# Kernel optimization log

Hardware: AMD Instinct MI355X
Metric: run time of the kernel (lower is better)

The kernel has to match this reference:

```python
import jax, jax.numpy as jnp
import numpy as np

DIM = 256      # channel dim
NW = 7         # n_win per side
HEADS = 8
TOPK = 4
KVW = 4        # kv_per_win (ada_avgpool output side)
EPS = 1e-6


def _dwconv(x, w, b):
    # depthwise conv, NHWC, 'SAME' == padding k//2 for odd kernels
    y = jax.lax.conv_general_dilated(
        x, w, (1, 1), 'SAME',
        dimension_numbers=('NHWC', 'HWIO', 'NHWC'),
        feature_group_count=x.shape[-1])
    return y + b


def _ln(x, g, b):
    mu = x.mean(-1, keepdims=True)
    var = ((x - mu) ** 2).mean(-1, keepdims=True)
    return (x - mu) * jax.lax.rsqrt(var + EPS) * g + b


def _bra(x, qkv_w, qkv_b, wo_w, wo_b, lepe_w, lepe_b):
    # BiLevelRoutingAttention, x: (n, H, W, C)
    n, H, W, C = x.shape
    hw, ww = H // NW, W // NW          # window size (8, 8)
    scale = C ** -0.5                   # qk_dim ** -0.5 (BiFormer uses full qk_dim)
    qkv = x @ qkv_w.T + qkv_b           # (n, H, W, 3C)
    # window partition: n (j hw) (i ww) c -> n (j i) hw ww c
    qkv_win = qkv.reshape(n, NW, hw, NW, ww, 3 * C)
    qkv_win = qkv_win.transpose(0, 1, 3, 2, 4, 5).reshape(n, NW * NW, hw, ww, 3 * C)
    q = qkv_win[..., :C]                # (n, p2, hw, ww, C)
    kv = qkv_win[..., C:]               # (n, p2, hw, ww, 2C)
    # --- window-level routing (q/k detached in torch; no fwd effect) ---
    q_win = q.mean((2, 3))              # (n, p2, C)
    k_win = kv[..., :C].mean((2, 3))    # (n, p2, C)
    logits = jnp.einsum('npc,nqc->npq', q_win * scale, k_win)
    _, idx = jax.lax.top_k(logits, TOPK)            # (n, p2, k)
    # --- kv downsample: adaptive avg pool (hw,ww)->(KVW,KVW), exact 2x2 mean here ---
    fh, fw = hw // KVW, ww // KVW
    kv_pix = kv.reshape(n, NW * NW, KVW, fh, KVW, fw, 2 * C).mean((3, 5))
    kv_pix = kv_pix.reshape(n, NW * NW, KVW * KVW, 2 * C)   # (n, p2, w2, 2C)
    # --- gather top-k windows' kv ---
    kv_sel = jax.vmap(lambda t, ix: t[ix])(kv_pix, idx)     # (n, p2, k, w2, 2C)
    cph = C // HEADS
    k_sel = kv_sel[..., :C].reshape(n, NW * NW, TOPK * KVW * KVW, HEADS, cph)
    v_sel = kv_sel[..., C:].reshape(n, NW * NW, TOPK * KVW * KVW, HEADS, cph)
    q_pix = q.reshape(n, NW * NW, hw * ww, HEADS, cph)
    # --- windowed attention over gathered tokens ---
    att = jnp.einsum('npqmc,npsmc->npmqs', q_pix * scale, k_sel)
    att = jax.nn.softmax(att, axis=-1)
    out = jnp.einsum('npmqs,npsmc->npqmc', att, v_sel)
    out = out.reshape(n, NW, NW, hw, ww, C).transpose(0, 1, 3, 2, 4, 5).reshape(n, H, W, C)
    # --- lepe: depthwise 5x5 on v over the full image ---
    v_img = qkv[..., 2 * C:]
    out = out + _dwconv(v_img, lepe_w, lepe_b)
    return out @ wo_w.T + wo_b


def setup_inputs() -> dict:
    key = jax.random.key(0)
    ks = jax.random.split(key, 8)
    C, s = DIM, 0.02
    p = {}
    p['x'] = jax.random.normal(ks[0], (16, C, 56, 56), jnp.float32)
    p['pos_w'] = jax.random.normal(ks[1], (3, 3, 1, C), jnp.float32) * s
    p['pos_b'] = jnp.zeros((C,), jnp.float32)
    p['ln1_g'] = jnp.ones((C,), jnp.float32)
    p['ln1_b'] = jnp.zeros((C,), jnp.float32)
    p['ln2_g'] = jnp.ones((C,), jnp.float32)
    p['ln2_b'] = jnp.zeros((C,), jnp.float32)
    p['qkv_w'] = jax.random.normal(ks[2], (3 * C, C), jnp.float32) * s
    p['qkv_b'] = jnp.zeros((3 * C,), jnp.float32)
    p['wo_w'] = jax.random.normal(ks[3], (C, C), jnp.float32) * s
    p['wo_b'] = jnp.zeros((C,), jnp.float32)
    p['lepe_w'] = jax.random.normal(ks[4], (5, 5, 1, C), jnp.float32) * s
    p['lepe_b'] = jnp.zeros((C,), jnp.float32)
    p['fc1_w'] = jax.random.normal(ks[5], (4 * C, C), jnp.float32) * s
    p['fc1_b'] = jnp.zeros((4 * C,), jnp.float32)
    p['fc2_w'] = jax.random.normal(ks[6], (C, 4 * C), jnp.float32) * s
    p['fc2_b'] = jnp.zeros((C,), jnp.float32)
    return p


def reference(x, pos_w, pos_b, ln1_g, ln1_b, ln2_g, ln2_b, qkv_w, qkv_b,
              wo_w, wo_b, lepe_w, lepe_b, fc1_w, fc1_b, fc2_w, fc2_b):
    xh = x.transpose(0, 2, 3, 1)                       # NCHW -> NHWC
    xh = xh + _dwconv(xh, pos_w, pos_b)                # pos embed (dw 3x3)
    xh = xh + _bra(_ln(xh, ln1_g, ln1_b), qkv_w, qkv_b, wo_w, wo_b, lepe_w, lepe_b)
    h = _ln(xh, ln2_g, ln2_b)
    h = jax.nn.gelu(h @ fc1_w.T + fc1_b, approximate=False)
    xh = xh + (h @ fc2_w.T + fc2_b)
    return xh.transpose(0, 3, 1, 2)                    # NHWC -> NCHW
```

## Files before the change

### kernel.cpp

```cpp
#include <hip/hip_runtime.h>
#include <math.h>

static constexpr int NIMG = 16;
static constexpr int TOK  = NIMG * 56 * 56;
static constexpr size_t TC = (size_t)TOK * 256;
static constexpr int PTOK = 784 * 16;

typedef __bf16 bf16x8 __attribute__((ext_vector_type(8)));
typedef float  f32x4  __attribute__((ext_vector_type(4)));

__device__ inline float bf2f(unsigned short u) {
  unsigned int i = ((unsigned int)u) << 16; float f; __builtin_memcpy(&f, &i, 4); return f;
}
__device__ inline unsigned short f2bf(float f) {
  unsigned int i; __builtin_memcpy(&i, &f, 4);
  unsigned int r = i + 0x7fffu + ((i >> 16) & 1u);
  return (unsigned short)(r >> 16);
}

__global__ __launch_bounds__(256) void nchw2nhwc(const float* __restrict__ x,
                                                 float* __restrict__ y) {
  __shared__ float T[32][37];
  int nh = blockIdx.z;
  int n = nh / 56, h = nh % 56;
  int c0 = blockIdx.y * 32, w0 = blockIdx.x * 32;
  int tid = threadIdx.x;
  int wlim = 56 - w0; if (wlim > 32) wlim = 32;
  {
    int ci = tid >> 3, w = (tid & 7) * 4;
    if (w < wlim) {
      f32x4 v = *(const f32x4*)&x[(((size_t)n * 256 + c0 + ci) * 56 + h) * 56 + w0 + w];
#pragma unroll
      for (int j = 0; j < 4; j++) T[ci][w + j] = v[j];
    }
  }
  __syncthreads();
  {
    int wi = tid >> 3, cq = tid & 7;
    if (wi < wlim) {
      f32x4 o;
#pragma unroll
      for (int k = 0; k < 4; k++) o[k] = T[cq * 4 + k][wi];
      *(f32x4*)&y[(((size_t)n * 56 + h) * 56 + w0 + wi) * 256 + c0 + cq * 4] = o;
    }
  }
}

__global__ __launch_bounds__(256) void nhwc2nchw(const float* __restrict__ y,
                                                 float* __restrict__ o) {
  __shared__ float T[32][37];
  int nh = blockIdx.z;
  int n = nh / 56, h = nh % 56;
  int w0 = blockIdx.x * 32, c0 = blockIdx.y * 32;
  int tid = threadIdx.x;
  int wlim = 56 - w0; if (wlim > 32) wlim = 32;
  {
    int wi = tid >> 3, cq = tid & 7;
    if (wi < wlim) {
      f32x4 v = *(const f32x4*)&y[(((size_t)n * 56 + h) * 56 + w0 + wi) * 256 + c0 + cq * 4];
#pragma unroll
      for (int k = 0; k < 4; k++) T[wi][cq * 4 + k] = v[k];
    }
  }
  __syncthreads();
  {
    int ci = tid >> 3, w = (tid & 7) * 4;
    if (w < wlim) {
      f32x4 ov;
#pragma unroll
      for (int j = 0; j < 4; j++) ov[j] = T[w + j][ci];
      *(f32x4*)&o[(((size_t)n * 256 + c0 + ci) * 56 + h) * 56 + w0 + w] = ov;
    }
  }
}

__global__ __launch_bounds__(256) void posln_kernel(const float* __restrict__ xt,
                                                    const float* __restrict__ w,
                                                    const float* __restrict__ bb,
                                                    const float* __restrict__ g1,
                                                    const float* __restrict__ b1,
                                                    float* __restrict__ xh,
                                                    unsigned short* __restrict__ lnb,
                                                    float* __restrict__ murs) {
  int bid = blockIdx.x;
  int wgid = (bid & 7) * 1568 + (bid >> 3);
  int t = wgid * 4 + (threadIdx.x >> 6);
  int lane = threadIdx.x & 63;
  int c = lane * 4;
  int n = t / 3136, rem = t % 3136, h = rem / 56, ww = rem % 56;
  const float* base = xt + (size_t)n * 3136 * 256 + c;

  f32x4 xx[9]; float msk[9];
#pragma unroll
  for (int k = 0; k < 9; k++) {
    int dh = k / 3 - 1, dw = k % 3 - 1;
    int hh = h + dh, wc = ww + dw;
    msk[k] = ((unsigned)hh < 56u && (unsigned)wc < 56u) ? 1.f : 0.f;
    int hcl = hh < 0 ? 0 : (hh > 55 ? 55 : hh);
    int wcl = wc < 0 ? 0 : (wc > 55 ? 55 : wc);
    xx[k] = *(const f32x4*)&base[(size_t)(hcl * 56 + wcl) * 256];
  }
  f32x4 acc = *(const f32x4*)&bb[c];
#pragma unroll
  for (int k = 0; k < 9; k++) {
    f32x4 wv = *(const f32x4*)&w[k * 256 + c];
    acc += xx[k] * (wv * msk[k]);
  }
  f32x4 v = xx[4] + acc;
  *(f32x4*)&xh[(size_t)t * 256 + c] = v;

  float s = v[0] + v[1] + v[2] + v[3];
#pragma unroll
  for (int m = 1; m < 64; m <<= 1) s += __shfl_xor(s, m);
  float mu = s * (1.f / 256.f);
  f32x4 d = v - mu;
  float ss = d[0] * d[0] + d[1] * d[1] + d[2] * d[2] + d[3] * d[3];
#pragma unroll
  for (int m = 1; m < 64; m <<= 1) ss += __shfl_xor(ss, m);
  float rs = rsqrtf(ss * (1.f / 256.f) + 1e-6f);
  f32x4 gg = *(const f32x4*)&g1[c];
  f32x4 b4 = *(const f32x4*)&b1[c];
  f32x4 y = d * rs * gg + b4;
  unsigned short yb[4];
#pragma unroll
  for (int j = 0; j < 4; j++) yb[j] = f2bf(y[j]);
  __builtin_memcpy(lnb + (size_t)t * 256 + c, yb, 8);
  if (lane == 0) {
    murs[2 * (size_t)t] = mu;
    murs[2 * (size_t)t + 1] = rs;
  }
}

template <bool OUTBF, bool LN2F>
__global__ __launch_bounds__(512, 4) void mgemm2(const unsigned short* __restrict__ A, int lda,
                                                 const unsigned short* __restrict__ B, int ldb,
                                                 const float* __restrict__ bias,
                                                 const float* __restrict__ R,
                                                 void* __restrict__ C_,
                                                 int N, int K, int flags, int gx,
                                                 const float* __restrict__ g2,
                                                 const float* __restrict__ b2,
                                                 unsigned short* __restrict__ ob2) {
  __shared__ __attribute__((aligned(16))) char smraw[49152];
  unsigned short* As = (unsigned short*)smraw;
  unsigned short* Bs = (unsigned short*)(smraw + 16384);
  float* slab = (float*)smraw;
  constexpr int SSTR = 260;

  int tid = threadIdx.x;
  int nwg = gridDim.x, bid = blockIdx.x;
  int q8 = nwg >> 3, r8 = nwg & 7;
  int xcd = bid & 7, pos = bid >> 3;
  int wgid = (xcd < r8 ? xcd * (q8 + 1) : r8 * (q8 + 1) + (xcd - r8) * q8) + pos;
  int m0 = (wgid / gx) * 128;
  int n0 = (wgid % gx) * 256;

  int lane = tid & 63, wid = tid >> 6;
  int wr = (wid >> 2) * 64, wc = (wid & 3) * 64;
  int llo = lane & 15, lhi = lane >> 4;

  f32x4 acc[4][4];
#pragma unroll
  for (int i = 0; i < 4; i++)
#pragma unroll
    for (int j = 0; j < 4; j++) acc[i][j] = (f32x4){0.f, 0.f, 0.f, 0.f};

  for (int k0 = 0; k0 < K; k0 += 64) {
#pragma unroll
    for (int i = 0; i < 2; i++) {
      int qa = tid + 512 * i;
      int row = qa >> 3, col = (qa & 7) ^ (row & 7);
      __builtin_amdgcn_global_load_lds(
          (const __attribute__((address_space(1))) unsigned int*)
              (A + (size_t)(m0 + row) * lda + k0 + col * 8),
          (__attribute__((address_space(3))) unsigned int*)(As + qa * 8), 16, 0, 0);
    }
#pragma unroll
    for (int i = 0; i < 4; i++) {
      int qb = tid + 512 * i;
      int row = qb >> 3, col = (qb & 7) ^ (row & 7);
      __builtin_amdgcn_global_load_lds(
          (const __attribute__((address_space(1))) unsigned int*)
              (B + (size_t)(n0 + row) * ldb + k0 + col * 8),
          (__attribute__((address_space(3))) unsigned int*)(Bs + qb * 8), 16, 0, 0);
    }
    __syncthreads();
#pragma unroll
    for (int ks = 0; ks < 2; ks++) {
      int cchunk = ks * 4 + lhi;
      bf16x8 af[4], bfr[4];
#pragma unroll
      for (int mi = 0; mi < 4; mi++) {
        int r = wr + mi * 16 + llo;
        __builtin_memcpy(&af[mi], As + (size_t)r * 64 + (cchunk ^ (r & 7)) * 8, 16);
      }
#pragma unroll
      for (int nj = 0; nj < 4; nj++) {
        int r = wc + nj * 16 + llo;
        __builtin_memcpy(&bfr[nj], Bs + (size_t)r * 64 + (cchunk ^ (r & 7)) * 8, 16);
      }
#pragma unroll
      for (int mi = 0; mi < 4; mi++)
#pragma unroll
        for (int nj = 0; nj < 4; nj++)
          acc[mi][nj] = __builtin_amdgcn_mfma_f32_16x16x32_bf16(af[mi], bfr[nj],
                                                                acc[mi][nj], 0, 0, 0);
    }
    __syncthreads();
  }

#pragma unroll
  for (int s = 0; s < 4; s++) {
    if (wr == (s >> 1) * 64) {
#pragma unroll
      for (int mi2 = 0; mi2 < 2; mi2++) {
        int mi = (s & 1) * 2 + mi2;
#pragma unroll
        for (int nj = 0; nj < 4; nj++) {
          int col = wc + nj * 16 + llo;
#pragma unroll
          for (int j = 0; j < 4; j++)
            slab[(mi2 * 16 + lhi * 4 + j) * SSTR + col] = acc[mi][nj][j];
        }
      }
    }
    __syncthreads();
    int gmBase = m0 + s * 32;
    if (OUTBF) {
#pragma unroll
      for (int i2 = 0; i2 < 2; i2++) {
        int rr = wid * 4 + i2 * 2 + (lane >> 5);
        int col = (lane & 31) * 8;
        f32x4 v0 = *(f32x4*)&slab[rr * SSTR + col];
        f32x4 v1 = *(f32x4*)&slab[rr * SSTR + col + 4];
        if (!(flags & 8)) {
          v0 += *(const f32x4*)&bias[n0 + col];
          v1 += *(const f32x4*)&bias[n0 + col + 4];
        }
        if (flags & 1) {
#pragma unroll
          for (int j = 0; j < 4; j++) {
            v0[j] = 0.5f * v0[j] * (1.0f + erff(v0[j] * 0.70710678118654752f));
            v1[j] = 0.5f * v1[j] * (1.0f + erff(v1[j] * 0.70710678118654752f));
          }
        }
        unsigned short ob[8];
#pragma unroll
        for (int j = 0; j < 4; j++) { ob[j] = f2bf(v0[j]); ob[4 + j] = f2bf(v1[j]); }
        __builtin_memcpy((unsigned short*)C_ + (size_t)(gmBase + rr) * N + n0 + col, ob, 16);
      }
    } else {
#pragma unroll
      for (int i = 0; i < 4; i++) {
        int rr = wid * 4 + i;
        int gm = gmBase + rr;
        int col = lane * 4;
        f32x4 v = *(f32x4*)&slab[rr * SSTR + col];
        if (!(flags & 8)) v += *(const f32x4*)&bias[n0 + col];
        if (flags & 1) {
#pragma unroll
          for (int j = 0; j < 4; j++)
            v[j] = 0.5f * v[j] * (1.0f + erff(v[j] * 0.70710678118654752f));
        }
        if (flags & 2) v += *(const f32x4*)&R[(size_t)gm * N + n0 + col];
        if (LN2F) {
          float sv = v[0] + v[1] + v[2] + v[3];
          float qv = v[0] * v[0] + v[1] * v[1] + v[2] * v[2] + v[3] * v[3];
#pragma unroll
          for (int d = 1; d < 64; d <<= 1) {
            sv += __shfl_xor(sv, d);
            qv += __shfl_xor(qv, d);
          }
          float mu = sv * (1.f / 256.f);
          float var = qv * (1.f / 256.f) - mu * mu;
          float rs = rsqrtf(var + 1e-6f);
          f32x4 g4 = *(const f32x4*)&g2[col];
          f32x4 b4 = *(const f32x4*)&b2[col];
          f32x4 y = (v - mu) * rs * g4 + b4;
          unsigned short yb[4];
#pragma unroll
          for (int j = 0; j < 4; j++) yb[j] = f2bf(y[j]);
          __builtin_memcpy(ob2 + (size_t)gm * 256 + col, yb, 8);
        }
        *(f32x4*)&((float*)C_)[(size_t)gm * N + n0 + col] = v;
      }
    }
    __syncthreads();
  }
}

__global__ __launch_bounds__(256) void prep_kernel(const float* __restrict__ qkv_w,
                                                   const float* __restrict__ qkv_b,
                                                   const float* __restrict__ wo_w,
                                                   const float* __restrict__ fc1_w,
                                                   const float* __restrict__ fc2_w,
                                                   const float* __restrict__ lepe_w,
                                                   unsigned short* __restrict__ wqv,
                                                   unsigned short* __restrict__ wkv,
                                                   unsigned short* __restrict__ wwo,
                                                   unsigned short* __restrict__ wfc1,
                                                   unsigned short* __restrict__ wfc2,
                                                   float* __restrict__ bqv,
                                                   unsigned short* __restrict__ wlep) {
  int i = blockIdx.x * 256 + threadIdx.x;
  if (i < 65536) { wqv[i] = f2bf(qkv_w[i]); }
  else if (i < 131072) { int j = i - 65536; wqv[65536 + j] = f2bf(qkv_w[512 * 256 + j]); }
  else if (i < 262144) { int j = i - 131072; wkv[j] = f2bf(qkv_w[256 * 256 + j]); }
  else if (i < 327680) { int j = i - 262144; wwo[j] = f2bf(wo_w[j]); }
  else if (i < 589824) { int j = i - 327680; wfc1[j] = f2bf(fc1_w[j]); }
  else if (i < 851968) { int j = i - 589824; wfc2[j] = f2bf(fc2_w[j]); }
  else if (i < 852480) { int j = i - 851968; bqv[j] = qkv_b[j < 256 ? j : j + 256]; }
  else if (i < 858880) { int j = i - 852480; wlep[j] = f2bf(lepe_w[j]); }
}

__global__ __launch_bounds__(256) void pool_kernel(const float* __restrict__ xh,
                                                   const float* __restrict__ murs,
                                                   const float* __restrict__ g1,
                                                   const float* __restrict__ b1,
                                                   unsigned short* __restrict__ plx,
                                                   float* __restrict__ wmx) {
  int np = blockIdx.x * 4 + (threadIdx.x >> 6);
  int lane = threadIdx.x & 63;
  int c = lane * 4;
  int n = np / 49, p = np % 49, wr = p / 7, wcq = p % 7;
  f32x4 g4 = *(const f32x4*)&g1[c];
  f32x4 b4 = *(const f32x4*)&b1[c];
  f32x4 tot = (f32x4){0.f, 0.f, 0.f, 0.f};
  for (int s = 0; s < 16; s++) {
    int i = s >> 2, j = s & 3;
    f32x4 z = (f32x4){0.f, 0.f, 0.f, 0.f};
    for (int di = 0; di < 2; di++)
      for (int dj = 0; dj < 2; dj++) {
        size_t t = ((size_t)n * 56 + wr * 8 + i * 2 + di) * 56 + wcq * 8 + j * 2 + dj;
        float mu = murs[2 * t], rs = murs[2 * t + 1];
        f32x4 v = *(const f32x4*)&xh[t * 256 + c];
        z += (v - mu) * rs;
      }
    z *= 0.25f;
    f32x4 cell = z * g4 + b4;
    unsigned short ab[4];
#pragma unroll
    for (int k = 0; k < 4; k++) ab[k] = f2bf(cell[k]);
    __builtin_memcpy(plx + ((size_t)np * 16 + s) * 256 + c, ab, 8);
    tot += z;
  }
  f32x4 wm = tot * (1.f / 16.f) * g4 + b4;
  *(f32x4*)&wmx[(size_t)np * 256 + c] = wm;
}

__global__ __launch_bounds__(256) void winproj_kernel(const float* __restrict__ wmx,
                                                      const float* __restrict__ qkv_w,
                                                      const float* __restrict__ qkv_b,
                                                      float* __restrict__ qkwin) {
  int np = blockIdx.x, t = threadIdx.x;
  __shared__ float xs[256];
  xs[t] = wmx[(size_t)np * 256 + t];
  __syncthreads();
  for (int rep = 0; rep < 2; rep++) {
    int n = t + rep * 256;
    const float* wrow = qkv_w + (size_t)n * 256;
    float s = qkv_b[n];
    for (int c = 0; c < 256; c++) s += xs[c] * wrow[c];
    qkwin[(size_t)np * 512 + n] = s;
  }
}

__global__ __launch_bounds__(64) void topk_kernel(const float* __restrict__ qkwin,
                                                  int* __restrict__ idx) {
  int np = blockIdx.x;
  int n = np / 49;
  int j = threadIdx.x;
  __shared__ float lg[49];
  if (j < 49) {
    const float* qp = qkwin + (size_t)np * 512;
    const float* kp = qkwin + ((size_t)n * 49 + j) * 512 + 256;
    float s = 0.f;
    for (int c = 0; c < 256; c++) s += qp[c] * kp[c];
    lg[j] = s;
  }
  __syncthreads();
  if (j == 0) {
    unsigned long long used = 0ull;
    for (int t = 0; t < 4; t++) {
      float best = -INFINITY;
      int bi = 0;
      for (int q = 0; q < 49; q++)
        if (!((used >> q) & 1ull) && lg[q] > best) { best = lg[q]; bi = q; }
      idx[np * 4 + t] = bi;
      used |= (1ull << bi);
    }
  }
}

__global__ __launch_bounds__(64) void attn_mfma(const unsigned short* __restrict__ qvb,
                                                const unsigned short* __restrict__ kvp,
                                                const int* __restrict__ idx,
                                                unsigned short* __restrict__ out) {
  __shared__ unsigned short Vt[32 * 72];
  __shared__ unsigned short Pl[64 * 72];
  int bid = blockIdx.x;
  int head = bid & 7, np = bid >> 3;
  int n = np / 49, p = np % 49;
  int h0 = (p / 7) * 8, w0 = (p % 7) * 8;
  int lane = threadIdx.x;
  int lhi = lane >> 4, llo = lane & 15;

  int wi4[4];
#pragma unroll
  for (int t = 0; t < 4; t++) wi4[t] = idx[np * 4 + t];

#pragma unroll
  for (int it = 0; it < 4; it++) {
    int cell = lane >> 2;
    int chunk = lane & 3;
    int s = it * 16 + cell;
    const unsigned short* g = kvp + ((size_t)(n * 49 + wi4[it]) * 16 + cell) * 512
                              + 256 + head * 32 + chunk * 8;
    unsigned short vv[8];
    __builtin_memcpy(vv, g, 16);
#pragma unroll
    for (int j = 0; j < 8; j++) Vt[(chunk * 8 + j) * 72 + s] = vv[j];
  }

  bf16x8 qf[4], kf[4];
#pragma unroll
  for (int mi = 0; mi < 4; mi++) {
    int row = mi * 16 + llo;
    int h = h0 + (row >> 3), w = w0 + (row & 7);
    __builtin_memcpy(&qf[mi],
                     qvb + (((size_t)n * 56 + h) * 56 + w) * 512 + head * 32 + lhi * 8, 16);
  }
#pragma unroll
  for (int nj = 0; nj < 4; nj++) {
    __builtin_memcpy(&kf[nj],
                     kvp + ((size_t)(n * 49 + wi4[nj]) * 16 + llo) * 512 + head * 32 + lhi * 8,
                     16);
  }

  f32x4 acc[4][4];
#pragma unroll
  for (int mi = 0; mi < 4; mi++)
#pragma unroll
    for (int nj = 0; nj < 4; nj++) acc[mi][nj] = (f32x4){0.f, 0.f, 0.f, 0.f};
#pragma unroll
  for (int mi = 0; mi < 4; mi++)
#pragma unroll
    for (int nj = 0; nj < 4; nj++)
      acc[mi][nj] = __builtin_amdgcn_mfma_f32_16x16x32_bf16(qf[mi], kf[nj], acc[mi][nj], 0, 0, 0);

#pragma unroll
  for (int mi = 0; mi < 4; mi++)
#pragma unroll
    for (int nj = 0; nj < 4; nj++) acc[mi][nj] *= 0.0625f;
#pragma unroll
  for (int mi = 0; mi < 4; mi++) {
#pragma unroll
    for (int reg = 0; reg < 4; reg++) {
      float m = fmaxf(fmaxf(acc[mi][0][reg], acc[mi][1][reg]),
                      fmaxf(acc[mi][2][reg], acc[mi][3][reg]));
      m = fmaxf(m, __shfl_xor(m, 1));
      m = fmaxf(m, __shfl_xor(m, 2));
      m = fmaxf(m, __shfl_xor(m, 4));
      m = fmaxf(m, __shfl_xor(m, 8));
      float sum = 0.f;
#pragma unroll
      for (int nj = 0; nj < 4; nj++) {
        float e = __expf(acc[mi][nj][reg] - m);
        acc[mi][nj][reg] = e;
        sum += e;
      }
      sum += __shfl_xor(sum, 1);
      sum += __shfl_xor(sum, 2);
      sum += __shfl_xor(sum, 4);
      sum += __shfl_xor(sum, 8);
      float inv = 1.0f / sum;
#pragma unroll
      for (int nj = 0; nj < 4; nj++) acc[mi][nj][reg] *= inv;
    }
  }

#pragma unroll
  for (int mi = 0; mi < 4; mi++)
#pragma unroll
    for (int nj = 0; nj < 4; nj++)
#pragma unroll
      for (int reg = 0; reg < 4; reg++) {
        int row = mi * 16 + lhi * 4 + reg;
        Pl[row * 72 + nj * 16 + llo] = f2bf(acc[mi][nj][reg]);
      }

  f32x4 o[4][2];
#pragma unroll
  for (int mi = 0; mi < 4; mi++)
#pragma unroll
    for (int nc = 0; nc < 2; nc++) o[mi][nc] = (f32x4){0.f, 0.f, 0.f, 0.f};
#pragma unroll
  for (int ks = 0; ks < 2; ks++) {
    bf16x8 pa[4], vb[2];
#pragma unroll
    for (int mi = 0; mi < 4; mi++)
      __builtin_memcpy(&pa[mi], Pl + (mi * 16 + llo) * 72 + ks * 32 + lhi * 8, 16);
#pragma unroll
    for (int nc = 0; nc < 2; nc++)
      __builtin_memcpy(&vb[nc], Vt + (nc * 16 + llo) * 72 + ks * 32 + lhi * 8, 16);
#pragma unroll
    for (int mi = 0; mi < 4; mi++)
#pragma unroll
      for (int nc = 0; nc < 2; nc++)
        o[mi][nc] = __builtin_amdgcn_mfma_f32_16x16x32_bf16(pa[mi], vb[nc], o[mi][nc], 0, 0, 0);
  }

  __syncthreads();
#pragma unroll
  for (int mi = 0; mi < 4; mi++)
#pragma unroll
    for (int nc = 0; nc < 2; nc++)
#pragma unroll
      for (int reg = 0; reg < 4; reg++) {
        int row = mi * 16 + lhi * 4 + reg;
        Pl[row * 40 + nc * 16 + llo] = f2bf(o[mi][nc][reg]);
      }
  __syncthreads();
#pragma unroll
  for (int it = 0; it < 4; it++) {
    int slot = it * 64 + lane;
    int row = slot >> 2, cp = slot & 3;
    unsigned short ov[8];
    __builtin_memcpy(ov, Pl + row * 40 + cp * 8, 16);
    int h = h0 + (row >> 3), w = w0 + (row & 7);
    __builtin_memcpy(out + (((size_t)n * 56 + h) * 56 + w) * 256 + head * 32 + cp * 8, ov, 16);
  }
}

__global__ __launch_bounds__(256) void lepe_kernel(const unsigned short* __restrict__ qvb,
                                                   const unsigned short* __restrict__ wlep,
                                                   const float* __restrict__ b,
                                                   unsigned short* __restrict__ out) {
  __shared__ unsigned short Vs[60 * 272];
  int bid = blockIdx.x;
  int wgid = (bid & 7) * 784 + (bid >> 3);
  int tb = wgid * 8;
  int n = tb / 3136, rem = tb % 3136;
  int h0 = rem / 56, w0 = rem % 56;
  int tid = threadIdx.x;

  const unsigned short* vimg = qvb + (size_t)n * 3136 * 512 + 256;
  {
    int chunk = tid & 31;
    for (int s = tid >> 5; s < 60; s += 8) {
      int r = s / 12, cc = s % 12;
      int hh = h0 + r - 2; hh = hh < 0 ? 0 : (hh > 55 ? 55 : hh);
      int wcg = w0 + cc - 2; wcg = wcg < 0 ? 0 : (wcg > 55 ? 55 : wcg);
      unsigned short tmp[8];
      __builtin_memcpy(tmp, vimg + (size_t)(hh * 56 + wcg) * 512 + chunk * 8, 16);
      __builtin_memcpy(&Vs[s * 272 + chunk * 8], tmp, 16);
    }
  }
  __syncthreads();

  int px = tid >> 5;
  int cg = tid & 31;
  int c = cg * 8;
  int wq = w0 + px;

  float acc[8];
#pragma unroll
  for (int j = 0; j < 8; j++) acc[j] = b[c + j];

#pragma unroll
  for (int r = 0; r < 5; r++) {
    float hok = ((unsigned)(h0 + r - 2) < 56u) ? 1.f : 0.f;
#pragma unroll
    for (int dc = 0; dc < 5; dc++) {
      float m = hok * (((unsigned)(wq + dc - 2) < 56u) ? 1.f : 0.f);
      int slot = r * 12 + px + dc;
      unsigned short vv[8], wv[8];
      __builtin_memcpy(vv, &Vs[slot * 272 + cg * 8], 16);
      __builtin_memcpy(wv, wlep + (r * 5 + dc) * 256 + c, 16);
#pragma unroll
      for (int j = 0; j < 8; j++) acc[j] += bf2f(vv[j]) * (bf2f(wv[j]) * m);
    }
  }

  size_t o = (size_t)(tb + px) * 256 + c;
  unsigned short ov[8];
  __builtin_memcpy(ov, out + o, 16);
  unsigned short nv[8];
#pragma unroll
  for (int j = 0; j < 8; j++) nv[j] = f2bf(bf2f(ov[j]) + acc[j]);
  __builtin_memcpy(out + o, nv, 16);
}

extern "C" void kernel_launch(void* const* d_in, const int* in_sizes, int n_in,
                              void* d_out, int out_size, void* d_ws, size_t ws_size,
                              hipStream_t stream) {
  const float* x      = (const float*)d_in[0];
  const float* pos_w  = (const float*)d_in[1];
  const float* pos_b  = (const float*)d_in[2];
  const float* ln1_g  = (const float*)d_in[3];
  const float* ln1_b  = (const float*)d_in[4];
  const float* ln2_g  = (const float*)d_in[5];
  const float* ln2_b  = (const float*)d_in[6];
  const float* qkv_w  = (const float*)d_in[7];
  const float* qkv_b  = (const float*)d_in[8];
  const float* wo_w   = (const float*)d_in[9];
  const float* wo_b   = (const float*)d_in[10];
  const float* lepe_w = (const float*)d_in[11];
  const float* lepe_b = (const float*)d_in[12];
  const float* fc1_w  = (const float*)d_in[13];
  const float* fc1_b  = (const float*)d_in[14];
  const float* fc2_w  = (const float*)d_in[15];
  const float* fc2_b  = (const float*)d_in[16];

  float*          xt   = (float*)d_out;
  unsigned short* qvb  = (unsigned short*)d_out;
  unsigned short* hbuf = (unsigned short*)d_out;

  float*          r2   = (float*)d_ws;
  float*          wmx  = r2 + TC;
  float*          qkw  = wmx + (size_t)784 * 256;
  float*          bqv  = qkw + (size_t)784 * 512;
  unsigned short* lnb  = (unsigned short*)(bqv + 512);
  unsigned short* aob  = lnb;
  unsigned short* ln2b = lnb;
  unsigned short* plx  = lnb + TC;
  unsigned short* kvp  = plx + (size_t)PTOK * 256;
  unsigned short* wqv  = kvp + (size_t)PTOK * 512;
  unsigned short* wkv  = wqv + (size_t)512 * 256;
  unsigned short* wwo  = wkv + (size_t)512 * 256;
  unsigned short* wfc1 = wwo + (size_t)256 * 256;
  unsigned short* wfc2 = wfc1 + (size_t)1024 * 256;
  int*            idx  = (int*)(wfc2 + (size_t)256 * 1024);
  float*          murs = (float*)(idx + 784 * 4);
  unsigned short* wlep = (unsigned short*)(murs + (size_t)TOK * 2);
  unsigned short* hfull = wlep + 6400;

  size_t base_bytes = (size_t)((char*)hfull - (char*)d_ws);
  bool fullmlp = ws_size >= base_bytes + (size_t)TOK * 1024 * 2;

  prep_kernel<<<3355, 256, 0, stream>>>(qkv_w, qkv_b, wo_w, fc1_w, fc2_w, lepe_w,
                                        wqv, wkv, wwo, wfc1, wfc2, bqv, wlep);
  nchw2nhwc<<<dim3(2, 8, NIMG * 56), 256, 0, stream>>>(x, xt);
  posln_kernel<<<TOK / 4, 256, 0, stream>>>(xt, pos_w, pos_b, ln1_g, ln1_b,
                                            r2, lnb, murs);
  pool_kernel<<<196, 256, 0, stream>>>(r2, murs, ln1_g, ln1_b, plx, wmx);
  mgemm2<true, false><<<784, 512, 0, stream>>>(lnb, 256, wqv, 256, bqv, nullptr,
                                               qvb, 512, 256, 0, 2,
                                               nullptr, nullptr, nullptr);
  mgemm2<true, false><<<196, 512, 0, stream>>>(plx, 256, wkv, 256, qkv_b + 256, nullptr,
                                               kvp, 512, 256, 0, 2,
                                               nullptr, nullptr, nullptr);
  winproj_kernel<<<784, 256, 0, stream>>>(wmx, qkv_w, qkv_b, qkw);
  topk_kernel<<<784, 64, 0, stream>>>(qkw, idx);
  attn_mfma<<<6272, 64, 0, stream>>>(qvb, kvp, idx, aob);
  lepe_kernel<<<TOK / 8, 256, 0, stream>>>(qvb, wlep, lepe_b, aob);
  mgemm2<false, true><<<392, 512, 0, stream>>>(aob, 256, wwo, 256, wo_b, r2,
                                               r2, 256, 256, 2, 1,
                                               ln2_g, ln2_b, ln2b);
  if (fullmlp) {
    mgemm2<true, false><<<1568, 512, 0, stream>>>(ln2b, 256, wfc1, 256, fc1_b, nullptr,
                                                  hfull, 1024, 256, 1, 4,
                                                  nullptr, nullptr, nullptr);
    mgemm2<false, false><<<392, 512, 0, stream>>>(hfull, 1024, wfc2, 1024, fc2_b, r2,
                                                  r2, 256, 1024, 2, 1,
                                                  nullptr, nullptr, nullptr);
  } else {
    mgemm2<true, false><<<784, 512, 0, stream>>>(ln2b, 256, wfc1, 256, fc1_b, nullptr,
                                                 hbuf, 512, 256, 1, 2,
                                                 nullptr, nullptr, nullptr);
    mgemm2<false, false><<<392, 512, 0, stream>>>(hbuf, 512, wfc2, 1024, fc2_b, r2,
                                                  r2, 256, 512, 2, 1,
                                                  nullptr, nullptr, nullptr);
    mgemm2<true, false><<<784, 512, 0, stream>>>(ln2b, 256, wfc1 + (size_t)512 * 256, 256,
                                                 fc1_b + 512, nullptr,
                                                 hbuf, 512, 256, 1, 2,
                                                 nullptr, nullptr, nullptr);
    mgemm2<false, false><<<392, 512, 0, stream>>>(hbuf, 512, wfc2 + 512, 1024, fc2_b, r2,
                                                  r2, 256, 512, 2 | 8, 1,
                                                  nullptr, nullptr, nullptr);
  }
  nhwc2nchw<<<dim3(2, 8, NIMG * 56), 256, 0, stream>>>(r2, (float*)d_out);
}
```

Baseline: 445.9 us.

## Fuse fc1+GELU+fc2 MLP and NCHW output transpose into one kernel

Replaces the separate fc1 GEMM, fc2 GEMM and final NHWC->NCHW transpose with a single kernel. For each 64-token tile it computes the hidden activations in 256-wide chunks, keeps them in LDS as bf16, and accumulates the fc2 output in registers. The epilogue adds bias and residual and writes directly in NCHW layout through an LDS slab. This removes the global round trip of the 1024-wide hidden tensor and a separate transpose pass. The cost is that fc1 work is split across sequential chunks in one block, with large LDS use (72KB), lower occupancy and no load/compute double buffering.

```diff
diff --git a/kernel.cpp b/kernel.cpp
--- a/kernel.cpp
+++ b/kernel.cpp
@@ -42,34 +42,6 @@
 #pragma unroll
       for (int k = 0; k < 4; k++) o[k] = T[cq * 4 + k][wi];
       *(f32x4*)&y[(((size_t)n * 56 + h) * 56 + w0 + wi) * 256 + c0 + cq * 4] = o;
-    }
-  }
-}
-
-__global__ __launch_bounds__(256) void nhwc2nchw(const float* __restrict__ y,
-                                                 float* __restrict__ o) {
-  __shared__ float T[32][37];
-  int nh = blockIdx.z;
-  int n = nh / 56, h = nh % 56;
-  int w0 = blockIdx.x * 32, c0 = blockIdx.y * 32;
-  int tid = threadIdx.x;
-  int wlim = 56 - w0; if (wlim > 32) wlim = 32;
-  {
-    int wi = tid >> 3, cq = tid & 7;
-    if (wi < wlim) {
-      f32x4 v = *(const f32x4*)&y[(((size_t)n * 56 + h) * 56 + w0 + wi) * 256 + c0 + cq * 4];
-#pragma unroll
-      for (int k = 0; k < 4; k++) T[wi][cq * 4 + k] = v[k];
-    }
-  }
-  __syncthreads();
-  {
-    int ci = tid >> 3, w = (tid & 7) * 4;
-    if (w < wlim) {
-      f32x4 ov;
-#pragma unroll
-      for (int j = 0; j < 4; j++) ov[j] = T[w + j][ci];
-      *(f32x4*)&o[(((size_t)n * 256 + c0 + ci) * 56 + h) * 56 + w0 + w] = ov;
     }
   }
 }
@@ -283,6 +255,181 @@
           __builtin_memcpy(ob2 + (size_t)gm * 256 + col, yb, 8);
         }
         *(f32x4*)&((float*)C_)[(size_t)gm * N + n0 + col] = v;
+      }
+    }
+    __syncthreads();
+  }
+}
+
+__global__ __launch_bounds__(256) void mlp_fused(const unsigned short* __restrict__ A,
+                                                 const unsigned short* __restrict__ W1,
+                                                 const float* __restrict__ b1,
+                                                 const unsigned short* __restrict__ W2,
+                                                 const float* __restrict__ b2,
+                                                 const float* __restrict__ R,
+                                                 float* __restrict__ outp) {
+  __shared__ __attribute__((aligned(16))) char sm[73728];
+  unsigned short* As = (unsigned short*)sm;
+  unsigned short* Bs = (unsigned short*)(sm + 8192);
+  unsigned short* Hs = (unsigned short*)(sm + 40960);
+  float* slab = (float*)sm;
+  constexpr int SSTR = 260;
+
+  int tid = threadIdx.x;
+  int m0 = blockIdx.x * 64;
+  int lane = tid & 63, wid = tid >> 6;
+  int wc = wid * 64;
+  int llo = lane & 15, lhi = lane >> 4;
+
+  f32x4 accC[4][4];
+#pragma unroll
+  for (int i = 0; i < 4; i++)
+#pragma unroll
+    for (int j = 0; j < 4; j++) accC[i][j] = (f32x4){0.f, 0.f, 0.f, 0.f};
+
+  for (int hc = 0; hc < 4; hc++) {
+    f32x4 acc[4][4];
+#pragma unroll
+    for (int i = 0; i < 4; i++)
+#pragma unroll
+      for (int j = 0; j < 4; j++) acc[i][j] = (f32x4){0.f, 0.f, 0.f, 0.f};
+
+    for (int ks = 0; ks < 4; ks++) {
+#pragma unroll
+      for (int i = 0; i < 2; i++) {
+        int q = tid + 256 * i;
+        int row = q >> 3, col = (q & 7) ^ (row & 7);
+        __builtin_amdgcn_global_load_lds(
+            (const __attribute__((address_space(1))) unsigned int*)
+                (A + (size_t)(m0 + row) * 256 + ks * 64 + col * 8),
+            (__attribute__((address_space(3))) unsigned int*)(As + q * 8), 16, 0, 0);
+      }
+#pragma unroll
+      for (int i = 0; i < 8; i++) {
+        int q = tid + 256 * i;
+        int row = q >> 3, col = (q & 7) ^ (row & 7);
+        __builtin_amdgcn_global_load_lds(
+            (const __attribute__((address_space(1))) unsigned int*)
+                (W1 + (size_t)(hc * 256 + row) * 256 + ks * 64 + col * 8),
+            (__attribute__((address_space(3))) unsigned int*)(Bs + q * 8), 16, 0, 0);
+      }
+      __syncthreads();
+#pragma unroll
+      for (int kh = 0; kh < 2; kh++) {
+        int cchunk = kh * 4 + lhi;
+        bf16x8 af[4], bfr[4];
+#pragma unroll
+        for (int mi = 0; mi < 4; mi++) {
+          int r = mi * 16 + llo;
+          __builtin_memcpy(&af[mi], As + (size_t)r * 64 + (cchunk ^ (r & 7)) * 8, 16);
+        }
+#pragma unroll
+        for (int nj = 0; nj < 4; nj++) {
+          int r = wc + nj * 16 + llo;
+          __builtin_memcpy(&bfr[nj], Bs + (size_t)r * 64 + (cchunk ^ (r & 7)) * 8, 16);
+        }
+#pragma unroll
+        for (int mi = 0; mi < 4; mi++)
+#pragma unroll
+          for (int nj = 0; nj < 4; nj++)
+            acc[mi][nj] = __builtin_amdgcn_mfma_f32_16x16x32_bf16(af[mi], bfr[nj],
+                                                                  acc[mi][nj], 0, 0, 0);
+      }
+      __syncthreads();
+    }
+
+#pragma unroll
+    for (int nj = 0; nj < 4; nj++) {
+      int col = wc + nj * 16 + llo;
+      float bv = b1[hc * 256 + col];
+      int chunk = col >> 3, lo = col & 7;
+#pragma unroll
+      for (int mi = 0; mi < 4; mi++)
+#pragma unroll
+        for (int j = 0; j < 4; j++) {
+          int row = mi * 16 + lhi * 4 + j;
+          float h = acc[mi][nj][j] + bv;
+          h = 0.5f * h * (1.0f + erff(h * 0.70710678118654752f));
+          int swz = (chunk & 24) | ((chunk & 7) ^ (row & 7));
+          Hs[(size_t)row * 256 + swz * 8 + lo] = f2bf(h);
+        }
+    }
+    __syncthreads();
+
+    for (int ks2 = 0; ks2 < 4; ks2++) {
+#pragma unroll
+      for (int i = 0; i < 8; i++) {
+        int q = tid + 256 * i;
+        int row = q >> 3, col = (q & 7) ^ (row & 7);
+        __builtin_amdgcn_global_load_lds(
+            (const __attribute__((address_space(1))) unsigned int*)
+                (W2 + (size_t)row * 1024 + hc * 256 + ks2 * 64 + col * 8),
+            (__attribute__((address_space(3))) unsigned int*)(Bs + q * 8), 16, 0, 0);
+      }
+      __syncthreads();
+#pragma unroll
+      for (int kh = 0; kh < 2; kh++) {
+        int cc = kh * 4 + lhi;
+        int chunk = ks2 * 8 + cc;
+        bf16x8 af[4], bfr[4];
+#pragma unroll
+        for (int mi = 0; mi < 4; mi++) {
+          int r = mi * 16 + llo;
+          int swz = (chunk & 24) | ((chunk & 7) ^ (r & 7));
+          __builtin_memcpy(&af[mi], Hs + (size_t)r * 256 + swz * 8, 16);
+        }
+#pragma unroll
+        for (int nj = 0; nj < 4; nj++) {
+          int r = wc + nj * 16 + llo;
+          __builtin_memcpy(&bfr[nj], Bs + (size_t)r * 64 + (cc ^ (r & 7)) * 8, 16);
+        }
+#pragma unroll
+        for (int mi = 0; mi < 4; mi++)
+#pragma unroll
+          for (int nj = 0; nj < 4; nj++)
+            accC[mi][nj] = __builtin_amdgcn_mfma_f32_16x16x32_bf16(af[mi], bfr[nj],
+                                                                   accC[mi][nj], 0, 0, 0);
+      }
+      __syncthreads();
+    }
+  }
+
+  int n_img = m0 / 3136;
+  int hwb = m0 % 3136;
+#pragma unroll
+  for (int s = 0; s < 2; s++) {
+#pragma unroll
+    for (int mi2 = 0; mi2 < 2; mi2++) {
+      int mi = s * 2 + mi2;
+#pragma unroll
+      for (int nj = 0; nj < 4; nj++) {
+        int col = wc + nj * 16 + llo;
+#pragma unroll
+        for (int j = 0; j < 4; j++)
+          slab[(mi2 * 16 + lhi * 4 + j) * SSTR + col] = accC[mi][nj][j];
+      }
+    }
+    __syncthreads();
+#pragma unroll
+    for (int i = 0; i < 8; i++) {
+      int task = tid + 256 * i;
+      int rr = task >> 6, colg = (task & 63) * 4;
+      f32x4 v = *(f32x4*)&slab[rr * SSTR + colg];
+      v += *(const f32x4*)&b2[colg];
+      v += *(const f32x4*)&R[(size_t)(m0 + s * 32 + rr) * 256 + colg];
+      *(f32x4*)&slab[rr * SSTR + colg] = v;
+    }
+    __syncthreads();
+    {
+      int c = tid;
+      float buf[32];
+#pragma unroll
+      for (int r = 0; r < 32; r++) buf[r] = slab[r * SSTR + c];
+      float* dst = outp + ((size_t)n_img * 256 + c) * 3136 + hwb + s * 32;
+#pragma unroll
+      for (int i = 0; i < 8; i++) {
+        f32x4 v = (f32x4){buf[i * 4], buf[i * 4 + 1], buf[i * 4 + 2], buf[i * 4 + 3]};
+        *(f32x4*)&dst[i * 4] = v;
       }
     }
     __syncthreads();
@@ -614,7 +761,6 @@
 
   float*          xt   = (float*)d_out;
   unsigned short* qvb  = (unsigned short*)d_out;
-  unsigned short* hbuf = (unsigned short*)d_out;
 
   float*          r2   = (float*)d_ws;
   float*          wmx  = r2 + TC;
@@ -633,10 +779,6 @@
   int*            idx  = (int*)(wfc2 + (size_t)256 * 1024);
   float*          murs = (float*)(idx + 784 * 4);
   unsigned short* wlep = (unsigned short*)(murs + (size_t)TOK * 2);
-  unsigned short* hfull = wlep + 6400;
-
-  size_t base_bytes = (size_t)((char*)hfull - (char*)d_ws);
-  bool fullmlp = ws_size >= base_bytes + (size_t)TOK * 1024 * 2;
 
   prep_kernel<<<3355, 256, 0, stream>>>(qkv_w, qkv_b, wo_w, fc1_w, fc2_w, lepe_w,
                                         wqv, wkv, wwo, wfc1, wfc2, bqv, wlep);
@@ -657,27 +799,6 @@
   mgemm2<false, true><<<392, 512, 0, stream>>>(aob, 256, wwo, 256, wo_b, r2,
                                                r2, 256, 256, 2, 1,
                                                ln2_g, ln2_b, ln2b);
-  if (fullmlp) {
-    mgemm2<true, false><<<1568, 512, 0, stream>>>(ln2b, 256, wfc1, 256, fc1_b, nullptr,
-                                                  hfull, 1024, 256, 1, 4,
-                                                  nullptr, nullptr, nullptr);
-    mgemm2<false, false><<<392, 512, 0, stream>>>(hfull, 1024, wfc2, 1024, fc2_b, r2,
-                                                  r2, 256, 1024, 2, 1,
-                                                  nullptr, nullptr, nullptr);
-  } else {
-    mgemm2<true, false><<<784, 512, 0, stream>>>(ln2b, 256, wfc1, 256, fc1_b, nullptr,
-                                                 hbuf, 512, 256, 1, 2,
-                                                 nullptr, nullptr, nullptr);
-    mgemm2<false, false><<<392, 512, 0, stream>>>(hbuf, 512, wfc2, 1024, fc2_b, r2,
-                                                  r2, 256, 512, 2, 1,
-                                                  nullptr, nullptr, nullptr);
-    mgemm2<true, false><<<784, 512, 0, stream>>>(ln2b, 256, wfc1 + (size_t)512 * 256, 256,
-                                                 fc1_b + 512, nullptr,
-                                                 hbuf, 512, 256, 1, 2,
-                                                 nullptr, nullptr, nullptr);
-    mgemm2<false, false><<<392, 512, 0, stream>>>(hbuf, 512, wfc2 + 512, 1024, fc2_b, r2,
-                                                  r2, 256, 512, 2 | 8, 1,
-                                                  nullptr, nullptr, nullptr);
-  }
-  nhwc2nchw<<<dim3(2, 8, NIMG * 56), 256, 0, stream>>>(r2, (float*)d_out);
-}
+  mlp_fused<<<TOK / 64, 256, 0, stream>>>(ln2b, wfc1, fc1_b, wfc2, fc2_b, r2,
+                                          (float*)d_out);
+}
```

After: 519.6 us. +16.5%, slower.
